# Performance work log

Hardware: AMD Instinct MI355X
Metric: run time of the kernel (lower is better)

## Reference

```python
import jax, jax.numpy as jnp
import numpy as np

N, C, H, W = 64, 3, 345, 456


def _gs_linspace(n):
    # torch affine_grid (align_corners=False) coordinate vector:
    # symmetric construction: forward linspace for i < n/2, mirrored for i >= n/2
    i = jnp.arange(n)
    step = 2.0 / n
    start = -(1.0 - 1.0 / n)
    fwd = i.astype(jnp.float32) * step + start
    bwd = -start - (n - 1 - i).astype(jnp.float32) * step
    return jnp.where(i < n / 2.0, fwd, bwd)


def setup_inputs() -> dict:
    key = jax.random.key(0)
    k1, k2 = jax.random.split(key)
    x = jax.random.normal(k1, (N, C, H, W), dtype=jnp.float32)
    eye = jnp.array([[1.0, 0.0, 0.0], [0.0, 1.0, 0.0]], dtype=jnp.float32)
    theta = jnp.tile(eye[None], (N, 1, 1)) + 0.1 * jax.random.normal(k2, (N, 2, 3), dtype=jnp.float32)
    return {"x": x, "theta": theta}


def _grid_sample_bilinear_zeros(x, theta):
    n, c, h, w = x.shape
    xs = _gs_linspace(w)                       # [W]
    ys = _gs_linspace(h)                       # [H]
    base = jnp.stack(
        [jnp.broadcast_to(xs[None, :], (h, w)),
         jnp.broadcast_to(ys[:, None], (h, w)),
         jnp.ones((h, w), jnp.float32)], axis=-1)          # [H,W,3]
    grid = jnp.einsum('hwk,nok->nhwo', base, theta)         # [N,H,W,2]
    # unnormalize (align_corners=False): ix = gx*W/2 + (W-1)/2
    ix = grid[..., 0] * (w / 2.0) + (w - 1) / 2.0
    iy = grid[..., 1] * (h / 2.0) + (h - 1) / 2.0
    x0 = jnp.floor(ix)
    y0 = jnp.floor(iy)
    x1 = x0 + 1.0
    y1 = y0 + 1.0

    def corner(xc, yc, wt):
        valid = (xc >= 0) & (xc < w) & (yc >= 0) & (yc < h)
        xi = jnp.where(valid, xc, 0.0).astype(jnp.int32)    # [N,H,W]
        yi = jnp.where(valid, yc, 0.0).astype(jnp.int32)
        wts = jnp.where(valid, wt, 0.0)
        # gather per batch: img[C,H,W], yi/xi [H,W] -> [C,H,W]
        vals = jax.vmap(lambda img, yy, xx: img[:, yy, xx])(x, yi, xi)  # [N,C,H,W]
        return vals * wts[:, None]

    out = (corner(x0, y0, (x1 - ix) * (y1 - iy))
           + corner(x1, y0, (ix - x0) * (y1 - iy))
           + corner(x0, y1, (x1 - ix) * (iy - y0))
           + corner(x1, y1, (ix - x0) * (iy - y0)))
    return out


def reference(x, theta):
    return _grid_sample_bilinear_zeros(x, theta)
```

## Files before the change

kernel.cpp:

```cpp
#include <hip/hip_runtime.h>

constexpr int N_ = 64, C_ = 3, H_ = 345, W_ = 456;
constexpr int HW_ = H_ * W_;

constexpr int TW = 32, TH = 16;
constexpr int TX = (W_ + TW - 1) / TW;
constexpr int TY = (H_ + TH - 1) / TH;
constexpr int TILES = TX * TY;
constexpr int CCAP = 52;
constexpr int RCAP = 28;
constexpr int CJ   = CCAP / 4;
constexpr int CH_STRIDE = RCAP * CCAP;

__global__ __launch_bounds__(256, 8) void gs_tiled(
    const float* __restrict__ x,
    const float* __restrict__ theta,
    float* __restrict__ out)
{
    __shared__ float lds[3 * CH_STRIDE];

    int b    = blockIdx.x;
    int xcd  = b & 7;
    int i    = b >> 3;
    int bg   = i / TILES;
    int tile = i - bg * TILES;
    int n    = xcd + 8 * bg;

    int ty = tile / TX;
    int tx = tile - ty * TX;
    int w0 = tx * TW, h0 = ty * TH;

    const float* t = theta + n * 6;
    float t00 = t[0], t01 = t[1], t02 = t[2];
    float t10 = t[3], t11 = t[4], t12 = t[5];

    const float halfW = 0.5f * (float)W_, cW = 0.5f * (float)(W_ - 1);
    const float halfH = 0.5f * (float)H_, cH = 0.5f * (float)(H_ - 1);
    const float startx = -(1.0f - 1.0f / (float)W_);
    const float starty = -(1.0f - 1.0f / (float)H_);

    float Ax = t00;
    float Bx = t01 * ((float)W_ / (float)H_);
    float Cx = fmaf(startx, t00, fmaf(starty, t01, t02)) * halfW + cW;
    float Ay = t10 * ((float)H_ / (float)W_);
    float By = t11;
    float Cy = fmaf(startx, t10, fmaf(starty, t11, t12)) * halfH + cH;

    float ws = (float)w0, we = (float)min(w0 + TW - 1, W_ - 1);
    float hs = (float)h0, he = (float)min(h0 + TH - 1, H_ - 1);

    float xw0 = ws * Ax, xw1 = we * Ax;
    float xh0 = hs * Bx, xh1 = he * Bx;
    float minix = Cx + fminf(xw0, xw1) + fminf(xh0, xh1);
    float maxix = Cx + fmaxf(xw0, xw1) + fmaxf(xh0, xh1);

    float yw0 = ws * Ay, yw1 = we * Ay;
    float yh0 = hs * By, yh1 = he * By;
    float miniy = Cy + fminf(yw0, yw1) + fminf(yh0, yh1);
    float maxiy = Cy + fmaxf(yw0, yw1) + fmaxf(yh0, yh1);

    int x_lo = (int)floorf(minix) - 1, x_hi = (int)floorf(maxix) + 2;
    int y_lo = (int)floorf(miniy) - 1, y_hi = (int)floorf(maxiy) + 2;

    int xa    = x_lo & ~3;
    int cols  = x_hi - xa + 1;
    int cols4 = (cols + 3) >> 2;
    if (cols4 > CJ) {
        xa += ((cols4 - CJ) >> 1) << 2;
        cols4 = CJ;
    }
    int colsp = cols4 << 2;
    int rows  = y_hi - y_lo + 1;
    if (rows > RCAP) {
        y_lo += (rows - RCAP) >> 1;
        rows = RCAP;
    }

    const float* xn = x + (size_t)n * 3 * HW_;
    int tid = threadIdx.x;

    {
        int j  = tid & 15;
        int rt = tid >> 4;
        if (j < cols4) {
            bool interior = (xa >= 0) && (xa + colsp <= W_) && (y_lo >= 0) && (y_lo + rows <= H_);
            if (interior) {
                #pragma unroll
                for (int c = 0; c < 3; ++c) {
                    const float* src = xn + c * HW_ + xa + 4 * j;
                    float* dst = &lds[c * CH_STRIDE + 4 * j];
                    for (int r = rt; r < rows; r += 16)
                        *(float4*)(dst + r * CCAP) = *(const float4*)(src + (size_t)(y_lo + r) * W_);
                }
            } else {
                int xc = xa + 4 * j;
                bool ok0 = (unsigned)(xc + 0) < (unsigned)W_;
                bool ok1 = (unsigned)(xc + 1) < (unsigned)W_;
                bool ok2 = (unsigned)(xc + 2) < (unsigned)W_;
                bool ok3 = (unsigned)(xc + 3) < (unsigned)W_;
                #pragma unroll
                for (int c = 0; c < 3; ++c) {
                    const float* src = xn + c * HW_;
                    float* dst = &lds[c * CH_STRIDE + 4 * j];
                    for (int r = rt; r < rows; r += 16) {
                        int y = y_lo + r;
                        bool yok = (unsigned)y < (unsigned)H_;
                        const float* row = src + (size_t)y * W_ + xc;
                        float4 v;
                        v.x = (yok && ok0) ? row[0] : 0.0f;
                        v.y = (yok && ok1) ? row[1] : 0.0f;
                        v.z = (yok && ok2) ? row[2] : 0.0f;
                        v.w = (yok && ok3) ? row[3] : 0.0f;
                        *(float4*)(dst + r * CCAP) = v;
                    }
                }
            }
        }
        __syncthreads();
    }

    int tw = (tid & 15) * 2, th = tid >> 4;
    int w = w0 + tw, h = h0 + th;
    if (w >= W_ || h >= H_) return;

    float fw = (float)w, fh = (float)h;
    float hx  = fmaf(fh, Bx, Cx), hy = fmaf(fh, By, Cy);
    float ixA = fmaf(fw, Ax, hx), iyA = fmaf(fw, Ay, hy);
    float ixB = ixA + Ax,         iyB = iyA + Ay;

    float xfA = floorf(ixA), yfA = floorf(iyA);
    float fxA = ixA - xfA,   fyA = iyA - yfA;
    int   XA  = (int)xfA,    YA  = (int)yfA;

    float xfB = floorf(ixB), yfB = floorf(iyB);
    float fxB = ixB - xfB,   fyB = iyB - yfB;
    int   XB  = (int)xfB,    YB  = (int)yfB;

    int lcA = XA - xa, lrA = YA - y_lo;
    int lcB = XB - xa, lrB = YB - y_lo;
    bool inA = (unsigned)lcA < (unsigned)(colsp - 1) && (unsigned)lrA < (unsigned)(rows - 1);
    bool inB = (unsigned)lcB < (unsigned)(colsp - 1) && (unsigned)lrB < (unsigned)(rows - 1);

    float vA0, vA1, vA2, vB0, vB1, vB2;

    if (__builtin_expect(inA & inB, 1)) {
        const float* pA = &lds[lrA * CCAP + lcA];
        const float* pB = &lds[lrB * CCAP + lcB];
        {
            float a00 = pA[0], a10 = pA[1], a01 = pA[CCAP], a11 = pA[CCAP + 1];
            float b00 = pB[0], b10 = pB[1], b01 = pB[CCAP], b11 = pB[CCAP + 1];
            float at = fmaf(fxA, a10 - a00, a00), ab = fmaf(fxA, a11 - a01, a01);
            float bt = fmaf(fxB, b10 - b00, b00), bb = fmaf(fxB, b11 - b01, b01);
            vA0 = fmaf(fyA, ab - at, at);
            vB0 = fmaf(fyB, bb - bt, bt);
        }
        {
            float a00 = pA[CH_STRIDE], a10 = pA[CH_STRIDE + 1];
            float a01 = pA[CH_STRIDE + CCAP], a11 = pA[CH_STRIDE + CCAP + 1];
            float b00 = pB[CH_STRIDE], b10 = pB[CH_STRIDE + 1];
            float b01 = pB[CH_STRIDE + CCAP], b11 = pB[CH_STRIDE + CCAP + 1];
            float at = fmaf(fxA, a10 - a00, a00), ab = fmaf(fxA, a11 - a01, a01);
            float bt = fmaf(fxB, b10 - b00, b00), bb = fmaf(fxB, b11 - b01, b01);
            vA1 = fmaf(fyA, ab - at, at);
            vB1 = fmaf(fyB, bb - bt, bt);
        }
        {
            float a00 = pA[2 * CH_STRIDE], a10 = pA[2 * CH_STRIDE + 1];
            float a01 = pA[2 * CH_STRIDE + CCAP], a11 = pA[2 * CH_STRIDE + CCAP + 1];
            float b00 = pB[2 * CH_STRIDE], b10 = pB[2 * CH_STRIDE + 1];
            float b01 = pB[2 * CH_STRIDE + CCAP], b11 = pB[2 * CH_STRIDE + CCAP + 1];
            float at = fmaf(fxA, a10 - a00, a00), ab = fmaf(fxA, a11 - a01, a01);
            float bt = fmaf(fxB, b10 - b00, b00), bb = fmaf(fxB, b11 - b01, b01);
            vA2 = fmaf(fyA, ab - at, at);
            vB2 = fmaf(fyB, bb - bt, bt);
        }
    } else {
        float gxA = 1.0f - fxA, gyA = 1.0f - fyA;
        float gxB = 1.0f - fxB, gyB = 1.0f - fyB;
        float wA00 = gxA * gyA, wA10 = fxA * gyA, wA01 = gxA * fyA, wA11 = fxA * fyA;
        float wB00 = gxB * gyB, wB10 = fxB * gyB, wB01 = gxB * fyB, wB11 = fxB * fyB;
        vA0 = vA1 = vA2 = vB0 = vB1 = vB2 = 0.0f;
#define CORNG(xi, yi, wt, d0, d1, d2)                                         \
        if ((unsigned)(xi) < (unsigned)W_ && (unsigned)(yi) < (unsigned)H_) { \
            int off = (yi) * W_ + (xi);                                       \
            d0 += xn[off] * (wt);                                             \
            d1 += xn[HW_ + off] * (wt);                                       \
            d2 += xn[2 * HW_ + off] * (wt);                                   \
        }
        CORNG(XA,     YA,     wA00, vA0, vA1, vA2)
        CORNG(XA + 1, YA,     wA10, vA0, vA1, vA2)
        CORNG(XA,     YA + 1, wA01, vA0, vA1, vA2)
        CORNG(XA + 1, YA + 1, wA11, vA0, vA1, vA2)
        CORNG(XB,     YB,     wB00, vB0, vB1, vB2)
        CORNG(XB + 1, YB,     wB10, vB0, vB1, vB2)
        CORNG(XB,     YB + 1, wB01, vB0, vB1, vB2)
        CORNG(XB + 1, YB + 1, wB11, vB0, vB1, vB2)
#undef CORNG
    }

    size_t o = (size_t)n * 3 * HW_ + (size_t)h * W_ + w;
    *(float2*)(out + o)           = make_float2(vA0, vB0);
    *(float2*)(out + o + HW_)     = make_float2(vA1, vB1);
    *(float2*)(out + o + 2 * HW_) = make_float2(vA2, vB2);
}

extern "C" void kernel_launch(void* const* d_in, const int* in_sizes, int n_in,
                              void* d_out, int out_size, void* d_ws, size_t ws_size,
                              hipStream_t stream) {
    const float* x     = (const float*)d_in[0];
    const float* theta = (const float*)d_in[1];
    float* out = (float*)d_out;

    int blocks = N_ * TILES;
    gs_tiled<<<blocks, 256, 0, stream>>>(x, theta, out);
}
```

Measured before the change: 46.72 us.

## Make blocks persistent over a tile column with register-prefetched LDS staging

Each block now walks about 5-6 vertically consecutive tiles of one tile column instead of handling a single tile. The next tile's input window is loaded into registers before the current tile is computed, then written to LDS after a barrier. The aim is to hide global load latency behind compute and to cut launch and per-block setup overhead. In exchange the grid shrinks from 21120 to 3840 blocks, there are two barriers per tile, and staging always loads a fixed 52x28 window, so register pressure and load volume go up.

```diff
diff --git a/kernel.cpp b/kernel.cpp
--- a/kernel.cpp
+++ b/kernel.cpp
@@ -4,13 +4,103 @@
 constexpr int HW_ = H_ * W_;
 
 constexpr int TW = 32, TH = 16;
-constexpr int TX = (W_ + TW - 1) / TW;
-constexpr int TY = (H_ + TH - 1) / TH;
-constexpr int TILES = TX * TY;
+constexpr int TX = 15, TY = 22;
+constexpr int QS = 4;
 constexpr int CCAP = 52;
 constexpr int RCAP = 28;
-constexpr int CJ   = CCAP / 4;
+constexpr int CJ   = 13;
 constexpr int CH_STRIDE = RCAP * CCAP;
+
+__device__ __forceinline__ void make_win(
+    int w0, int h0, float Ax, float Bx, float Cx, float Ay, float By, float Cy,
+    int& xa_out, int& ylo_out)
+{
+    float ws = (float)w0, we = (float)min(w0 + TW - 1, W_ - 1);
+    float hs = (float)h0, he = (float)min(h0 + TH - 1, H_ - 1);
+    float xw0 = ws * Ax, xw1 = we * Ax;
+    float xh0 = hs * Bx, xh1 = he * Bx;
+    float minix = Cx + fminf(xw0, xw1) + fminf(xh0, xh1);
+    float maxix = Cx + fmaxf(xw0, xw1) + fmaxf(xh0, xh1);
+    float yw0 = ws * Ay, yw1 = we * Ay;
+    float yh0 = hs * By, yh1 = he * By;
+    float miniy = Cy + fminf(yw0, yw1) + fminf(yh0, yh1);
+    float maxiy = Cy + fmaxf(yw0, yw1) + fmaxf(yh0, yh1);
+
+    int x_lo = (int)floorf(minix) - 1, x_hi = (int)floorf(maxix) + 2;
+    int y_lo = (int)floorf(miniy) - 1, y_hi = (int)floorf(maxiy) + 2;
+
+    int xa = x_lo & ~3;
+    int cols4 = (x_hi - xa + 4) >> 2;
+    if (cols4 > CJ) xa += ((cols4 - CJ) >> 1) << 2;
+    int rows = y_hi - y_lo + 1;
+    if (rows > RCAP) y_lo += (rows - RCAP) >> 1;
+
+    xa_out = xa; ylo_out = y_lo;
+}
+
+__device__ __forceinline__ void stage_load(
+    const float* __restrict__ xn, int xa, int ylo, int j, int rt, bool lo2,
+    float4& s00, float4& s01, float4& s10, float4& s11, float4& s20, float4& s21)
+{
+    if (j >= CJ) return;
+    int y0 = ylo + rt;
+    bool interior = (xa >= 0) && (xa + CCAP <= W_) && (ylo >= 0) && (ylo + RCAP <= H_);
+    if (interior) {
+        const float* p0 = xn + (size_t)y0 * W_ + xa + 4 * j;
+        s00 = *(const float4*)(p0);
+        s10 = *(const float4*)(p0 + HW_);
+        s20 = *(const float4*)(p0 + 2 * HW_);
+        if (lo2) {
+            const float* p1 = p0 + 16 * W_;
+            s01 = *(const float4*)(p1);
+            s11 = *(const float4*)(p1 + HW_);
+            s21 = *(const float4*)(p1 + 2 * HW_);
+        }
+    } else {
+        int xc = xa + 4 * j;
+        bool ok0 = (unsigned)(xc + 0) < (unsigned)W_;
+        bool ok1 = (unsigned)(xc + 1) < (unsigned)W_;
+        bool ok2 = (unsigned)(xc + 2) < (unsigned)W_;
+        bool ok3 = (unsigned)(xc + 3) < (unsigned)W_;
+        auto ld = [&](const float* src, int y) -> float4 {
+            bool yok = (unsigned)y < (unsigned)H_;
+            const float* row = src + (size_t)y * W_ + xc;
+            float4 v;
+            v.x = (yok && ok0) ? row[0] : 0.0f;
+            v.y = (yok && ok1) ? row[1] : 0.0f;
+            v.z = (yok && ok2) ? row[2] : 0.0f;
+            v.w = (yok && ok3) ? row[3] : 0.0f;
+            return v;
+        };
+        s00 = ld(xn, y0);
+        s10 = ld(xn + HW_, y0);
+        s20 = ld(xn + 2 * HW_, y0);
+        if (lo2) {
+            int y1 = y0 + 16;
+            s01 = ld(xn, y1);
+            s11 = ld(xn + HW_, y1);
+            s21 = ld(xn + 2 * HW_, y1);
+        }
+    }
+}
+
+__device__ __forceinline__ void stage_write(
+    float* lds, int j, int rt, bool lo2,
+    const float4& s00, const float4& s01, const float4& s10,
+    const float4& s11, const float4& s20, const float4& s21)
+{
+    if (j >= CJ) return;
+    float* d0 = lds + rt * CCAP + 4 * j;
+    *(float4*)(d0)                 = s00;
+    *(float4*)(d0 + CH_STRIDE)     = s10;
+    *(float4*)(d0 + 2 * CH_STRIDE) = s20;
+    if (lo2) {
+        float* d1 = d0 + 16 * CCAP;
+        *(float4*)(d1)                 = s01;
+        *(float4*)(d1 + CH_STRIDE)     = s11;
+        *(float4*)(d1 + 2 * CH_STRIDE) = s21;
+    }
+}
 
 __global__ __launch_bounds__(256, 8) void gs_tiled(
     const float* __restrict__ x,
@@ -22,13 +112,14 @@
     int b    = blockIdx.x;
     int xcd  = b & 7;
     int i    = b >> 3;
-    int bg   = i / TILES;
-    int tile = i - bg * TILES;
+    int bg   = i / (TX * QS);
+    int rem  = i - bg * (TX * QS);
+    int tx   = rem >> 2;
+    int q    = rem & 3;
     int n    = xcd + 8 * bg;
-
-    int ty = tile / TX;
-    int tx = tile - ty * TX;
-    int w0 = tx * TW, h0 = ty * TH;
+    int ty0  = (q * TY) >> 2;
+    int ty1  = ((q + 1) * TY) >> 2;
+    int w0   = tx * TW;
 
     const float* t = theta + n * 6;
     float t00 = t[0], t01 = t[1], t02 = t[2];
@@ -46,162 +137,121 @@
     float By = t11;
     float Cy = fmaf(startx, t10, fmaf(starty, t11, t12)) * halfH + cH;
 
-    float ws = (float)w0, we = (float)min(w0 + TW - 1, W_ - 1);
-    float hs = (float)h0, he = (float)min(h0 + TH - 1, H_ - 1);
-
-    float xw0 = ws * Ax, xw1 = we * Ax;
-    float xh0 = hs * Bx, xh1 = he * Bx;
-    float minix = Cx + fminf(xw0, xw1) + fminf(xh0, xh1);
-    float maxix = Cx + fmaxf(xw0, xw1) + fmaxf(xh0, xh1);
-
-    float yw0 = ws * Ay, yw1 = we * Ay;
-    float yh0 = hs * By, yh1 = he * By;
-    float miniy = Cy + fminf(yw0, yw1) + fminf(yh0, yh1);
-    float maxiy = Cy + fmaxf(yw0, yw1) + fmaxf(yh0, yh1);
-
-    int x_lo = (int)floorf(minix) - 1, x_hi = (int)floorf(maxix) + 2;
-    int y_lo = (int)floorf(miniy) - 1, y_hi = (int)floorf(maxiy) + 2;
-
-    int xa    = x_lo & ~3;
-    int cols  = x_hi - xa + 1;
-    int cols4 = (cols + 3) >> 2;
-    if (cols4 > CJ) {
-        xa += ((cols4 - CJ) >> 1) << 2;
-        cols4 = CJ;
-    }
-    int colsp = cols4 << 2;
-    int rows  = y_hi - y_lo + 1;
-    if (rows > RCAP) {
-        y_lo += (rows - RCAP) >> 1;
-        rows = RCAP;
-    }
-
     const float* xn = x + (size_t)n * 3 * HW_;
+    float* on = out + (size_t)n * 3 * HW_;
+
     int tid = threadIdx.x;
-
-    {
-        int j  = tid & 15;
-        int rt = tid >> 4;
-        if (j < cols4) {
-            bool interior = (xa >= 0) && (xa + colsp <= W_) && (y_lo >= 0) && (y_lo + rows <= H_);
-            if (interior) {
-                #pragma unroll
-                for (int c = 0; c < 3; ++c) {
-                    const float* src = xn + c * HW_ + xa + 4 * j;
-                    float* dst = &lds[c * CH_STRIDE + 4 * j];
-                    for (int r = rt; r < rows; r += 16)
-                        *(float4*)(dst + r * CCAP) = *(const float4*)(src + (size_t)(y_lo + r) * W_);
+    int j  = tid & 15, rt = tid >> 4;
+    bool lo2 = rt < 12;
+    int tw = (tid & 15) * 2, th = tid >> 4;
+
+    float4 s00 = {}, s01 = {}, s10 = {}, s11 = {}, s20 = {}, s21 = {};
+
+    int cxa, cylo;
+    make_win(w0, ty0 * TH, Ax, Bx, Cx, Ay, By, Cy, cxa, cylo);
+    stage_load(xn, cxa, cylo, j, rt, lo2, s00, s01, s10, s11, s20, s21);
+    stage_write(lds, j, rt, lo2, s00, s01, s10, s11, s20, s21);
+    __syncthreads();
+
+    for (int k = ty0; k < ty1; ++k) {
+        bool hn = (k + 1) < ty1;
+        int nxa = 0, nylo = 0;
+        if (hn) {
+            make_win(w0, (k + 1) * TH, Ax, Bx, Cx, Ay, By, Cy, nxa, nylo);
+            stage_load(xn, nxa, nylo, j, rt, lo2, s00, s01, s10, s11, s20, s21);
+        }
+
+        int h = k * TH + th;
+        int w = w0 + tw;
+        if (w < W_ && h < H_) {
+            float fw = (float)w, fh = (float)h;
+            float hx  = fmaf(fh, Bx, Cx), hy = fmaf(fh, By, Cy);
+            float ixA = fmaf(fw, Ax, hx), iyA = fmaf(fw, Ay, hy);
+            float ixB = ixA + Ax,         iyB = iyA + Ay;
+
+            float xfA = floorf(ixA), yfA = floorf(iyA);
+            float fxA = ixA - xfA,   fyA = iyA - yfA;
+            int   XA  = (int)xfA,    YA  = (int)yfA;
+
+            float xfB = floorf(ixB), yfB = floorf(iyB);
+            float fxB = ixB - xfB,   fyB = iyB - yfB;
+            int   XB  = (int)xfB,    YB  = (int)yfB;
+
+            int lcA = XA - cxa, lrA = YA - cylo;
+            int lcB = XB - cxa, lrB = YB - cylo;
+            bool inA = (unsigned)lcA < (unsigned)(CCAP - 1) && (unsigned)lrA < (unsigned)(RCAP - 1);
+            bool inB = (unsigned)lcB < (unsigned)(CCAP - 1) && (unsigned)lrB < (unsigned)(RCAP - 1);
+
+            float vA0, vA1, vA2, vB0, vB1, vB2;
+
+            if (__builtin_expect(inA & inB, 1)) {
+                const float* pA = &lds[lrA * CCAP + lcA];
+                const float* pB = &lds[lrB * CCAP + lcB];
+                {
+                    float a00 = pA[0], a10 = pA[1], a01 = pA[CCAP], a11 = pA[CCAP + 1];
+                    float b00 = pB[0], b10 = pB[1], b01 = pB[CCAP], b11 = pB[CCAP + 1];
+                    float at = fmaf(fxA, a10 - a00, a00), ab = fmaf(fxA, a11 - a01, a01);
+                    float bt = fmaf(fxB, b10 - b00, b00), bb = fmaf(fxB, b11 - b01, b01);
+                    vA0 = fmaf(fyA, ab - at, at);
+                    vB0 = fmaf(fyB, bb - bt, bt);
+                }
+                {
+                    float a00 = pA[CH_STRIDE], a10 = pA[CH_STRIDE + 1];
+                    float a01 = pA[CH_STRIDE + CCAP], a11 = pA[CH_STRIDE + CCAP + 1];
+                    float b00 = pB[CH_STRIDE], b10 = pB[CH_STRIDE + 1];
+                    float b01 = pB[CH_STRIDE + CCAP], b11 = pB[CH_STRIDE + CCAP + 1];
+                    float at = fmaf(fxA, a10 - a00, a00), ab = fmaf(fxA, a11 - a01, a01);
+                    float bt = fmaf(fxB, b10 - b00, b00), bb = fmaf(fxB, b11 - b01, b01);
+                    vA1 = fmaf(fyA, ab - at, at);
+                    vB1 = fmaf(fyB, bb - bt, bt);
+                }
+                {
+                    float a00 = pA[2 * CH_STRIDE], a10 = pA[2 * CH_STRIDE + 1];
+                    float a01 = pA[2 * CH_STRIDE + CCAP], a11 = pA[2 * CH_STRIDE + CCAP + 1];
+                    float b00 = pB[2 * CH_STRIDE], b10 = pB[2 * CH_STRIDE + 1];
+                    float b01 = pB[2 * CH_STRIDE + CCAP], b11 = pB[2 * CH_STRIDE + CCAP + 1];
+                    float at = fmaf(fxA, a10 - a00, a00), ab = fmaf(fxA, a11 - a01, a01);
+                    float bt = fmaf(fxB, b10 - b00, b00), bb = fmaf(fxB, b11 - b01, b01);
+                    vA2 = fmaf(fyA, ab - at, at);
+                    vB2 = fmaf(fyB, bb - bt, bt);
                 }
             } else {
-                int xc = xa + 4 * j;
-                bool ok0 = (unsigned)(xc + 0) < (unsigned)W_;
-                bool ok1 = (unsigned)(xc + 1) < (unsigned)W_;
-                bool ok2 = (unsigned)(xc + 2) < (unsigned)W_;
-                bool ok3 = (unsigned)(xc + 3) < (unsigned)W_;
-                #pragma unroll
-                for (int c = 0; c < 3; ++c) {
-                    const float* src = xn + c * HW_;
-                    float* dst = &lds[c * CH_STRIDE + 4 * j];
-                    for (int r = rt; r < rows; r += 16) {
-                        int y = y_lo + r;
-                        bool yok = (unsigned)y < (unsigned)H_;
-                        const float* row = src + (size_t)y * W_ + xc;
-                        float4 v;
-                        v.x = (yok && ok0) ? row[0] : 0.0f;
-                        v.y = (yok && ok1) ? row[1] : 0.0f;
-                        v.z = (yok && ok2) ? row[2] : 0.0f;
-                        v.w = (yok && ok3) ? row[3] : 0.0f;
-                        *(float4*)(dst + r * CCAP) = v;
-                    }
-                }
+                float gxA = 1.0f - fxA, gyA = 1.0f - fyA;
+                float gxB = 1.0f - fxB, gyB = 1.0f - fyB;
+                float wA00 = gxA * gyA, wA10 = fxA * gyA, wA01 = gxA * fyA, wA11 = fxA * fyA;
+                float wB00 = gxB * gyB, wB10 = fxB * gyB, wB01 = gxB * fyB, wB11 = fxB * fyB;
+                vA0 = vA1 = vA2 = vB0 = vB1 = vB2 = 0.0f;
+#define CORNG(xi, yi, wt, d0, d1, d2)                                         \
+                if ((unsigned)(xi) < (unsigned)W_ && (unsigned)(yi) < (unsigned)H_) { \
+                    int off = (yi) * W_ + (xi);                               \
+                    d0 += xn[off] * (wt);                                     \
+                    d1 += xn[HW_ + off] * (wt);                               \
+                    d2 += xn[2 * HW_ + off] * (wt);                           \
+                }
+                CORNG(XA,     YA,     wA00, vA0, vA1, vA2)
+                CORNG(XA + 1, YA,     wA10, vA0, vA1, vA2)
+                CORNG(XA,     YA + 1, wA01, vA0, vA1, vA2)
+                CORNG(XA + 1, YA + 1, wA11, vA0, vA1, vA2)
+                CORNG(XB,     YB,     wB00, vB0, vB1, vB2)
+                CORNG(XB + 1, YB,     wB10, vB0, vB1, vB2)
+                CORNG(XB,     YB + 1, wB01, vB0, vB1, vB2)
+                CORNG(XB + 1, YB + 1, wB11, vB0, vB1, vB2)
+#undef CORNG
             }
+
+            size_t o = (size_t)h * W_ + w;
+            *(float2*)(on + o)           = make_float2(vA0, vB0);
+            *(float2*)(on + o + HW_)     = make_float2(vA1, vB1);
+            *(float2*)(on + o + 2 * HW_) = make_float2(vA2, vB2);
+        }
+
+        __syncthreads();
+        if (hn) {
+            stage_write(lds, j, rt, lo2, s00, s01, s10, s11, s20, s21);
+            cxa = nxa; cylo = nylo;
         }
         __syncthreads();
     }
-
-    int tw = (tid & 15) * 2, th = tid >> 4;
-    int w = w0 + tw, h = h0 + th;
-    if (w >= W_ || h >= H_) return;
-
-    float fw = (float)w, fh = (float)h;
-    float hx  = fmaf(fh, Bx, Cx), hy = fmaf(fh, By, Cy);
-    float ixA = fmaf(fw, Ax, hx), iyA = fmaf(fw, Ay, hy);
-    float ixB = ixA + Ax,         iyB = iyA + Ay;
-
-    float xfA = floorf(ixA), yfA = floorf(iyA);
-    float fxA = ixA - xfA,   fyA = iyA - yfA;
-    int   XA  = (int)xfA,    YA  = (int)yfA;
-
-    float xfB = floorf(ixB), yfB = floorf(iyB);
-    float fxB = ixB - xfB,   fyB = iyB - yfB;
-    int   XB  = (int)xfB,    YB  = (int)yfB;
-
-    int lcA = XA - xa, lrA = YA - y_lo;
-    int lcB = XB - xa, lrB = YB - y_lo;
-    bool inA = (unsigned)lcA < (unsigned)(colsp - 1) && (unsigned)lrA < (unsigned)(rows - 1);
-    bool inB = (unsigned)lcB < (unsigned)(colsp - 1) && (unsigned)lrB < (unsigned)(rows - 1);
-
-    float vA0, vA1, vA2, vB0, vB1, vB2;
-
-    if (__builtin_expect(inA & inB, 1)) {
-        const float* pA = &lds[lrA * CCAP + lcA];
-        const float* pB = &lds[lrB * CCAP + lcB];
-        {
-            float a00 = pA[0], a10 = pA[1], a01 = pA[CCAP], a11 = pA[CCAP + 1];
-            float b00 = pB[0], b10 = pB[1], b01 = pB[CCAP], b11 = pB[CCAP + 1];
-            float at = fmaf(fxA, a10 - a00, a00), ab = fmaf(fxA, a11 - a01, a01);
-            float bt = fmaf(fxB, b10 - b00, b00), bb = fmaf(fxB, b11 - b01, b01);
-            vA0 = fmaf(fyA, ab - at, at);
-            vB0 = fmaf(fyB, bb - bt, bt);
-        }
-        {
-            float a00 = pA[CH_STRIDE], a10 = pA[CH_STRIDE + 1];
-            float a01 = pA[CH_STRIDE + CCAP], a11 = pA[CH_STRIDE + CCAP + 1];
-            float b00 = pB[CH_STRIDE], b10 = pB[CH_STRIDE + 1];
-            float b01 = pB[CH_STRIDE + CCAP], b11 = pB[CH_STRIDE + CCAP + 1];
-            float at = fmaf(fxA, a10 - a00, a00), ab = fmaf(fxA, a11 - a01, a01);
-            float bt = fmaf(fxB, b10 - b00, b00), bb = fmaf(fxB, b11 - b01, b01);
-            vA1 = fmaf(fyA, ab - at, at);
-            vB1 = fmaf(fyB, bb - bt, bt);
-        }
-        {
-            float a00 = pA[2 * CH_STRIDE], a10 = pA[2 * CH_STRIDE + 1];
-            float a01 = pA[2 * CH_STRIDE + CCAP], a11 = pA[2 * CH_STRIDE + CCAP + 1];
-            float b00 = pB[2 * CH_STRIDE], b10 = pB[2 * CH_STRIDE + 1];
-            float b01 = pB[2 * CH_STRIDE + CCAP], b11 = pB[2 * CH_STRIDE + CCAP + 1];
-            float at = fmaf(fxA, a10 - a00, a00), ab = fmaf(fxA, a11 - a01, a01);
-            float bt = fmaf(fxB, b10 - b00, b00), bb = fmaf(fxB, b11 - b01, b01);
-            vA2 = fmaf(fyA, ab - at, at);
-            vB2 = fmaf(fyB, bb - bt, bt);
-        }
-    } else {
-        float gxA = 1.0f - fxA, gyA = 1.0f - fyA;
-        float gxB = 1.0f - fxB, gyB = 1.0f - fyB;
-        float wA00 = gxA * gyA, wA10 = fxA * gyA, wA01 = gxA * fyA, wA11 = fxA * fyA;
-        float wB00 = gxB * gyB, wB10 = fxB * gyB, wB01 = gxB * fyB, wB11 = fxB * fyB;
-        vA0 = vA1 = vA2 = vB0 = vB1 = vB2 = 0.0f;
-#define CORNG(xi, yi, wt, d0, d1, d2)                                         \
-        if ((unsigned)(xi) < (unsigned)W_ && (unsigned)(yi) < (unsigned)H_) { \
-            int off = (yi) * W_ + (xi);                                       \
-            d0 += xn[off] * (wt);                                             \
-            d1 += xn[HW_ + off] * (wt);                                       \
-            d2 += xn[2 * HW_ + off] * (wt);                                   \
-        }
-        CORNG(XA,     YA,     wA00, vA0, vA1, vA2)
-        CORNG(XA + 1, YA,     wA10, vA0, vA1, vA2)
-        CORNG(XA,     YA + 1, wA01, vA0, vA1, vA2)
-        CORNG(XA + 1, YA + 1, wA11, vA0, vA1, vA2)
-        CORNG(XB,     YB,     wB00, vB0, vB1, vB2)
-        CORNG(XB + 1, YB,     wB10, vB0, vB1, vB2)
-        CORNG(XB,     YB + 1, wB01, vB0, vB1, vB2)
-        CORNG(XB + 1, YB + 1, wB11, vB0, vB1, vB2)
-#undef CORNG
-    }
-
-    size_t o = (size_t)n * 3 * HW_ + (size_t)h * W_ + w;
-    *(float2*)(out + o)           = make_float2(vA0, vB0);
-    *(float2*)(out + o + HW_)     = make_float2(vA1, vB1);
-    *(float2*)(out + o + 2 * HW_) = make_float2(vA2, vB2);
 }
 
 extern "C" void kernel_launch(void* const* d_in, const int* in_sizes, int n_in,
@@ -211,6 +261,6 @@
     const float* theta = (const float*)d_in[1];
     float* out = (float*)d_out;
 
-    int blocks = N_ * TILES;
+    int blocks = N_ * TX * QS;
     gs_tiled<<<blocks, 256, 0, stream>>>(x, theta, out);
 }
```

Result: slower. 136.0 us (+191.1%).
